# Performance work log

Hardware: AMD Instinct MI355X
Metric: run time of the kernel (lower is better)

## Reference

```python
import jax, jax.numpy as jnp
import numpy as np

M, L = 256, 256
E_EDGES = L - 1
EPS = 1e-12
HX, HZ, JZ = 3.0, 0.25, -1.0


def setup_inputs() -> dict:
    key = jax.random.key(0)
    k1, k2 = jax.random.split(key, 2)
    # original: uniform(-pi/2, pi/2); narrowed to keep cos(theta_m - theta_b) away from 0
    theta = jax.random.uniform(k1, (M, L), minval=-0.3, maxval=0.3, dtype=jnp.float32)
    coef = jax.random.uniform(k2, (M,), minval=-1.0, maxval=1.0, dtype=jnp.float32)
    edges_u = jnp.arange(E_EDGES, dtype=jnp.int32)       # 1D chain
    edges_v = edges_u + 1
    strengths = jnp.ones((E_EDGES,), dtype=jnp.float32)
    return {"theta": theta, "coef": coef, "edges_u": edges_u,
            "edges_v": edges_v, "strengths": strengths}


def reference(theta, coef, edges_u, edges_v, strengths):
    # theta: [M, L], coef: [M]
    cos_m = jnp.cos(theta)
    sin_m = jnp.sin(theta)
    cm = cos_m[:, None, :]   # [M,1,L] -> row m
    sm = sin_m[:, None, :]
    cb = cos_m[None, :, :]   # [1,M,L] -> row b
    sb = sin_m[None, :, :]
    # pairwise angle-sum/difference trig, all [M, M, L]
    cosd = cm * cb + sm * sb            # cos(theta_m - theta_b)
    sind = sm * cb - cm * sb            # sin(theta_m - theta_b)
    sins = sm * cb + cm * sb            # sin(theta_m + theta_b)
    coss = cm * cb - sm * sb            # cos(theta_m + theta_b)
    inv = 1.0 / (cosd + EPS)

    P = jnp.prod(cosd, axis=-1)                     # [M,M] overlap products
    U = jnp.sum(sins * inv, axis=-1)                # [M,M] sigma_x amplitude ratios
    V = jnp.sum(coss * inv, axis=-1)                # [M,M] sigma_z amplitude ratios
    a = coss * inv                                  # [M,M,L] per-site z ratio

    # ZZ interaction over graph edges
    Szz = jnp.einsum('e,mbe->mb', strengths,
                     a[:, :, edges_u] * a[:, :, edges_v])  # [M,M]

    F_total = HZ * V + HX * U + JZ * Szz            # [M,M]
    base = coef[:, None] * coef[None, :] * P        # [M,M]
    N = jnp.sum(base * F_total)
    D = jnp.sum(base)

    cP = coef[None, :] * P                          # c_b * P
    dN_dc = 2.0 * jnp.sum(cP * F_total, axis=1)     # [M]
    dD_dc = 2.0 * jnp.sum(cP, axis=1)               # [M]

    g_d = -sind * inv                               # d log cosd / d theta_mq
    Gxz = (-HZ * sins + HX * coss) * inv + (HZ * coss + HX * sins) * (sind * inv * inv)

    # incident-edge neighbor sums: inc[m,b,q] = sum_{e incident to q} s_e * a[m,b,nbr]
    uu = jnp.concatenate([edges_u, edges_v])
    vv = jnp.concatenate([edges_v, edges_u])
    ss = jnp.concatenate([strengths, strengths])
    inc = jnp.zeros_like(a).at[:, :, uu].add(ss * a[:, :, vv])
    Gzz = (-sins * inv + coss * (sind * inv * inv)) * inc * JZ

    w = base[:, :, None]                            # [M,M,1]
    dD_dtheta = 2.0 * jnp.sum(w * g_d, axis=1)      # [M,L]
    dN_dtheta = 2.0 * jnp.sum(
        w * (g_d * F_total[:, :, None] + Gxz + Gzz), axis=1)  # [M,L]

    E = N / D
    dE_dc = (dN_dc - E * dD_dc) / D
    dE_dtheta = (dN_dtheta - E * dD_dtheta) / D
    return dE_dtheta, dE_dc, E / L
```

## Files before the change

kernel.cpp:

```cpp
#include <hip/hip_runtime.h>
#include <math.h>

#define HXc 3.0f
#define HZc 0.25f
#define JZc (-1.0f)

#define OFF_COSR 0
#define OFF_SINR 65536
#define OFF_COST 131072
#define OFF_SINT 196608
#define OFF_DNT  262144
#define OFF_DDT  327680
#define OFF_NM   393216
#define OFF_DM   393472
#define OFF_CN   393728
#define OFF_CD   393984

__global__ __launch_bounds__(256) void k_prep(const float* __restrict__ theta,
                                              float* __restrict__ ws) {
    int i = blockIdx.x * 256 + threadIdx.x;
    float s, c;
    sincosf(theta[i], &s, &c);
    int m = i >> 8, l = i & 255;
    ws[OFF_COSR + i] = c;
    ws[OFF_SINR + i] = s;
    ws[OFF_COST + l * 256 + m] = c;
    ws[OFF_SINT + l * 256 + m] = s;
}

__global__ __launch_bounds__(1024) void k_main(
        const float* __restrict__ coef,
        const float* __restrict__ strengths,
        const float* __restrict__ cosR, const float* __restrict__ sinR,
        const float* __restrict__ cosT, const float* __restrict__ sinT,
        float* __restrict__ dNT, float* __restrict__ dDT,
        float* __restrict__ Nm, float* __restrict__ Dm,
        float* __restrict__ cN, float* __restrict__ cD) {
    int m = blockIdx.x;
    int tid = threadIdx.x;
    float coefm = coef[m];

    __shared__ float sLDS[256];
    __shared__ float4 quart[4][256];
    __shared__ float Flds[256], cPlds[256];
    __shared__ float wr[4][4];
    __shared__ float gN[16 * 256];
    __shared__ float gD[16 * 256];

    if (tid < 256) sLDS[tid] = (tid < 255) ? strengths[tid] : 0.0f;
    __syncthreads();

    {
        int b = tid & 255, q = tid >> 8;
        int l0 = q * 64;
        float p = 1.0f, u = 0.0f, v = 0.0f, z = 0.0f, a_prev = 0.0f;
        if (q) {
            int l = l0 - 1;
            float cmv = cosT[l * 256 + m], smv = sinT[l * 256 + m];
            float cbv = cosT[l * 256 + b], sbv = sinT[l * 256 + b];
            float t1 = cmv * cbv, t2 = smv * sbv;
            a_prev = (t1 - t2) * __builtin_amdgcn_rcpf(t1 + t2);
        }
        for (int l = l0; l < l0 + 64; ++l) {
            float cmv = cosT[l * 256 + m], smv = sinT[l * 256 + m];
            float cbv = cosT[l * 256 + b], sbv = sinT[l * 256 + b];
            float t1 = cmv * cbv, t2 = smv * sbv;
            float t3 = smv * cbv, t4 = cmv * sbv;
            float cosd = t1 + t2;
            float coss = t1 - t2;
            float sins = t3 + t4;
            float inv = __builtin_amdgcn_rcpf(cosd);
            p *= cosd;
            u = fmaf(sins, inv, u);
            v = fmaf(coss, inv, v);
            float a = coss * inv;
            float sPrev = (l > 0) ? sLDS[l - 1] : 0.0f;
            z = fmaf(sPrev * a_prev, a, z);
            a_prev = a;
        }
        quart[q][b] = make_float4(p, u, v, z);
    }
    __syncthreads();

    if (tid < 256) {
        float4 A = quart[0][tid], B = quart[1][tid];
        float4 C = quart[2][tid], Dq = quart[3][tid];
        float P = A.x * B.x * C.x * Dq.x;
        float U = A.y + B.y + C.y + Dq.y;
        float V = A.z + B.z + C.z + Dq.z;
        float Z = A.w + B.w + C.w + Dq.w;
        float F = HZc * V + HXc * U + JZc * Z;
        float cP = coef[tid] * P;
        Flds[tid] = F;
        cPlds[tid] = cP;
        float base = coefm * cP;
        float s1 = base, s2 = base * F, s3 = cP, s4 = cP * F;
        for (int o = 32; o; o >>= 1) {
            s1 += __shfl_xor(s1, o);
            s2 += __shfl_xor(s2, o);
            s3 += __shfl_xor(s3, o);
            s4 += __shfl_xor(s4, o);
        }
        if ((tid & 63) == 0) {
            int w = tid >> 6;
            wr[w][0] = s1; wr[w][1] = s2; wr[w][2] = s3; wr[w][3] = s4;
        }
    }
    __syncthreads();
    if (tid == 0) {
        Dm[m] = wr[0][0] + wr[1][0] + wr[2][0] + wr[3][0];
        Nm[m] = wr[0][1] + wr[1][1] + wr[2][1] + wr[3][1];
        cD[m] = wr[0][2] + wr[1][2] + wr[2][2] + wr[3][2];
        cN[m] = wr[0][3] + wr[1][3] + wr[2][3] + wr[3][3];
    }

    int w = tid >> 6, lane = tid & 63;
    int l0 = lane * 4;
    float4 cm4 = *(const float4*)&cosR[m * 256 + l0];
    float4 sm4 = *(const float4*)&sinR[m * 256 + l0];
    float cmv[4] = {cm4.x, cm4.y, cm4.z, cm4.w};
    float smv[4] = {sm4.x, sm4.y, sm4.z, sm4.w};
    float sR[4], sL[4];
#pragma unroll
    for (int j = 0; j < 4; ++j) {
        int l = l0 + j;
        sR[j] = sLDS[l];
        sL[j] = (l > 0) ? sLDS[l - 1] : 0.0f;
    }
    float pN[4] = {0.f, 0.f, 0.f, 0.f};
    float pD[4] = {0.f, 0.f, 0.f, 0.f};

    for (int i = 0; i < 16; ++i) {
        int b = w * 16 + i;
        float4 cb4 = *(const float4*)&cosR[b * 256 + l0];
        float4 sb4 = *(const float4*)&sinR[b * 256 + l0];
        float cbv[4] = {cb4.x, cb4.y, cb4.z, cb4.w};
        float sbv[4] = {sb4.x, sb4.y, sb4.z, sb4.w};
        float Fv = Flds[b];
        float base = coefm * cPlds[b];

        float a[4], inv[4], coss[4], sins[4], sind[4];
#pragma unroll
        for (int j = 0; j < 4; ++j) {
            float t1 = cmv[j] * cbv[j], t2 = smv[j] * sbv[j];
            float t3 = smv[j] * cbv[j], t4 = cmv[j] * sbv[j];
            float cosd = t1 + t2;
            coss[j] = t1 - t2;
            sins[j] = t3 + t4;
            sind[j] = t3 - t4;
            inv[j] = __builtin_amdgcn_rcpf(cosd);
            a[j] = coss[j] * inv[j];
        }
        float aLn = __shfl_up(a[3], 1);
        if (lane == 0) aLn = 0.0f;
        float aRn = __shfl_down(a[0], 1);
        if (lane == 63) aRn = 0.0f;
        float am1[4] = {aLn, a[0], a[1], a[2]};
        float ap1[4] = {a[1], a[2], a[3], aRn};
#pragma unroll
        for (int j = 0; j < 4; ++j) {
            float sii = sind[j] * inv[j];
            float g_d = -sii;
            float Gxz = (HXc * coss[j] - HZc * sins[j]) * inv[j]
                      + (HZc * coss[j] + HXc * sins[j]) * (sii * inv[j]);
            float K = JZc * ((coss[j] * sii - sins[j]) * inv[j]);
            float inc = fmaf(sR[j], ap1[j], sL[j] * am1[j]);
            float term = fmaf(Fv, g_d, fmaf(K, inc, Gxz));
            pN[j] = fmaf(base, term, pN[j]);
            pD[j] = fmaf(base, g_d, pD[j]);
        }
    }

    ((float4*)gN)[w * 64 + lane] = make_float4(pN[0], pN[1], pN[2], pN[3]);
    ((float4*)gD)[w * 64 + lane] = make_float4(pD[0], pD[1], pD[2], pD[3]);
    __syncthreads();
    if (tid < 256) {
        float sn = 0.0f, sd = 0.0f;
#pragma unroll
        for (int ww = 0; ww < 16; ++ww) {
            sn += gN[ww * 256 + tid];
            sd += gD[ww * 256 + tid];
        }
        dNT[m * 256 + tid] = sn;
        dDT[m * 256 + tid] = sd;
    }
}

__global__ __launch_bounds__(256) void k_fin(const float* __restrict__ ws,
                                             float* __restrict__ out) {
    int m = blockIdx.x, t = threadIdx.x;
    float nv = ws[OFF_NM + t], dv = ws[OFF_DM + t];
    for (int o = 32; o; o >>= 1) {
        nv += __shfl_xor(nv, o);
        dv += __shfl_xor(dv, o);
    }
    __shared__ float rn[4], rd[4];
    if ((t & 63) == 0) { rn[t >> 6] = nv; rd[t >> 6] = dv; }
    __syncthreads();
    float N = rn[0] + rn[1] + rn[2] + rn[3];
    float D = rd[0] + rd[1] + rd[2] + rd[3];
    float E = N / D;
    float invD = 1.0f / D;
    int i = m * 256 + t;
    out[i] = 2.0f * invD * (ws[OFF_DNT + i] - E * ws[OFF_DDT + i]);
    if (t == 0) out[65536 + m] = 2.0f * invD * (ws[OFF_CN + m] - E * ws[OFF_CD + m]);
    if (m == 0 && t == 1) out[65792] = E * (1.0f / 256.0f);
}

extern "C" void kernel_launch(void* const* d_in, const int* in_sizes, int n_in,
                              void* d_out, int out_size, void* d_ws, size_t ws_size,
                              hipStream_t stream) {
    const float* theta = (const float*)d_in[0];
    const float* coef = (const float*)d_in[1];
    const float* strengths = (const float*)d_in[4];
    float* out = (float*)d_out;
    float* ws = (float*)d_ws;

    k_prep<<<256, 256, 0, stream>>>(theta, ws);
    k_main<<<256, 1024, 0, stream>>>(coef, strengths,
                                     ws + OFF_COSR, ws + OFF_SINR,
                                     ws + OFF_COST, ws + OFF_SINT,
                                     ws + OFF_DNT, ws + OFF_DDT,
                                     ws + OFF_NM, ws + OFF_DM,
                                     ws + OFF_CN, ws + OFF_CD);
    k_fin<<<256, 256, 0, stream>>>(ws, out);
}
```

Baseline: 98.48 us.

## Fuse prep, main and finalize kernels into one cooperative kernel with grid syncs

Merges the three launches (sincos prep, main pairwise accumulation, final normalisation) into a single cooperative kernel that uses grid.sync between phases. Per-block gradient partials and c-gradient scalars now stay in LDS instead of round-tripping through workspace. This removes two kernel launch gaps and some global traffic. In exchange it adds the cost of grid-wide barriers and requires all 256 blocks of 1024 threads to be co-resident. It also reuses a = coss*inv for the V sum.

```diff
diff --git a/kernel.cpp b/kernel.cpp
--- a/kernel.cpp
+++ b/kernel.cpp
@@ -1,5 +1,8 @@
 #include <hip/hip_runtime.h>
+#include <hip/hip_cooperative_groups.h>
 #include <math.h>
+
+namespace cg = cooperative_groups;
 
 #define HXc 3.0f
 #define HZc 0.25f
@@ -9,36 +12,26 @@
 #define OFF_SINR 65536
 #define OFF_COST 131072
 #define OFF_SINT 196608
-#define OFF_DNT  262144
-#define OFF_DDT  327680
-#define OFF_NM   393216
-#define OFF_DM   393472
-#define OFF_CN   393728
-#define OFF_CD   393984
-
-__global__ __launch_bounds__(256) void k_prep(const float* __restrict__ theta,
-                                              float* __restrict__ ws) {
-    int i = blockIdx.x * 256 + threadIdx.x;
-    float s, c;
-    sincosf(theta[i], &s, &c);
-    int m = i >> 8, l = i & 255;
-    ws[OFF_COSR + i] = c;
-    ws[OFF_SINR + i] = s;
-    ws[OFF_COST + l * 256 + m] = c;
-    ws[OFF_SINT + l * 256 + m] = s;
-}
-
-__global__ __launch_bounds__(1024) void k_main(
+#define OFF_NM   262144
+#define OFF_DM   262400
+
+__global__ __launch_bounds__(1024) void k_all(
+        const float* __restrict__ theta,
         const float* __restrict__ coef,
         const float* __restrict__ strengths,
-        const float* __restrict__ cosR, const float* __restrict__ sinR,
-        const float* __restrict__ cosT, const float* __restrict__ sinT,
-        float* __restrict__ dNT, float* __restrict__ dDT,
-        float* __restrict__ Nm, float* __restrict__ Dm,
-        float* __restrict__ cN, float* __restrict__ cD) {
+        float* __restrict__ ws,
+        float* __restrict__ out) {
+    cg::grid_group grid = cg::this_grid();
+
     int m = blockIdx.x;
     int tid = threadIdx.x;
-    float coefm = coef[m];
+
+    float* __restrict__ cosR = ws + OFF_COSR;
+    float* __restrict__ sinR = ws + OFF_SINR;
+    float* __restrict__ cosT = ws + OFF_COST;
+    float* __restrict__ sinT = ws + OFF_SINT;
+    float* __restrict__ Nm = ws + OFF_NM;
+    float* __restrict__ Dm = ws + OFF_DM;
 
     __shared__ float sLDS[256];
     __shared__ float4 quart[4][256];
@@ -46,9 +39,20 @@
     __shared__ float wr[4][4];
     __shared__ float gN[16 * 256];
     __shared__ float gD[16 * 256];
-
-    if (tid < 256) sLDS[tid] = (tid < 255) ? strengths[tid] : 0.0f;
-    __syncthreads();
+    __shared__ float snL[256], sdL[256];
+    __shared__ float scal[4];
+
+    if (tid < 256) {
+        sLDS[tid] = (tid < 255) ? strengths[tid] : 0.0f;
+        int i = m * 256 + tid;
+        float s, c;
+        sincosf(theta[i], &s, &c);
+        cosR[i] = c;
+        sinR[i] = s;
+        cosT[tid * 256 + m] = c;
+        sinT[tid * 256 + m] = s;
+    }
+    grid.sync();
 
     {
         int b = tid & 255, q = tid >> 8;
@@ -72,8 +76,8 @@
             float inv = __builtin_amdgcn_rcpf(cosd);
             p *= cosd;
             u = fmaf(sins, inv, u);
-            v = fmaf(coss, inv, v);
             float a = coss * inv;
+            v += a;
             float sPrev = (l > 0) ? sLDS[l - 1] : 0.0f;
             z = fmaf(sPrev * a_prev, a, z);
             a_prev = a;
@@ -93,6 +97,7 @@
         float cP = coef[tid] * P;
         Flds[tid] = F;
         cPlds[tid] = cP;
+        float coefm = coef[m];
         float base = coefm * cP;
         float s1 = base, s2 = base * F, s3 = cP, s4 = cP * F;
         for (int o = 32; o; o >>= 1) {
@@ -110,69 +115,71 @@
     if (tid == 0) {
         Dm[m] = wr[0][0] + wr[1][0] + wr[2][0] + wr[3][0];
         Nm[m] = wr[0][1] + wr[1][1] + wr[2][1] + wr[3][1];
-        cD[m] = wr[0][2] + wr[1][2] + wr[2][2] + wr[3][2];
-        cN[m] = wr[0][3] + wr[1][3] + wr[2][3] + wr[3][3];
-    }
-
-    int w = tid >> 6, lane = tid & 63;
-    int l0 = lane * 4;
-    float4 cm4 = *(const float4*)&cosR[m * 256 + l0];
-    float4 sm4 = *(const float4*)&sinR[m * 256 + l0];
-    float cmv[4] = {cm4.x, cm4.y, cm4.z, cm4.w};
-    float smv[4] = {sm4.x, sm4.y, sm4.z, sm4.w};
-    float sR[4], sL[4];
-#pragma unroll
-    for (int j = 0; j < 4; ++j) {
-        int l = l0 + j;
-        sR[j] = sLDS[l];
-        sL[j] = (l > 0) ? sLDS[l - 1] : 0.0f;
-    }
-    float pN[4] = {0.f, 0.f, 0.f, 0.f};
-    float pD[4] = {0.f, 0.f, 0.f, 0.f};
-
-    for (int i = 0; i < 16; ++i) {
-        int b = w * 16 + i;
-        float4 cb4 = *(const float4*)&cosR[b * 256 + l0];
-        float4 sb4 = *(const float4*)&sinR[b * 256 + l0];
-        float cbv[4] = {cb4.x, cb4.y, cb4.z, cb4.w};
-        float sbv[4] = {sb4.x, sb4.y, sb4.z, sb4.w};
-        float Fv = Flds[b];
-        float base = coefm * cPlds[b];
-
-        float a[4], inv[4], coss[4], sins[4], sind[4];
+        scal[1] = wr[0][2] + wr[1][2] + wr[2][2] + wr[3][2];
+        scal[0] = wr[0][3] + wr[1][3] + wr[2][3] + wr[3][3];
+    }
+
+    {
+        int w = tid >> 6, lane = tid & 63;
+        int l0 = lane * 4;
+        float coefm = coef[m];
+        float4 cm4 = *(const float4*)&cosR[m * 256 + l0];
+        float4 sm4 = *(const float4*)&sinR[m * 256 + l0];
+        float cmv[4] = {cm4.x, cm4.y, cm4.z, cm4.w};
+        float smv[4] = {sm4.x, sm4.y, sm4.z, sm4.w};
+        float sR[4], sL[4];
 #pragma unroll
         for (int j = 0; j < 4; ++j) {
-            float t1 = cmv[j] * cbv[j], t2 = smv[j] * sbv[j];
-            float t3 = smv[j] * cbv[j], t4 = cmv[j] * sbv[j];
-            float cosd = t1 + t2;
-            coss[j] = t1 - t2;
-            sins[j] = t3 + t4;
-            sind[j] = t3 - t4;
-            inv[j] = __builtin_amdgcn_rcpf(cosd);
-            a[j] = coss[j] * inv[j];
-        }
-        float aLn = __shfl_up(a[3], 1);
-        if (lane == 0) aLn = 0.0f;
-        float aRn = __shfl_down(a[0], 1);
-        if (lane == 63) aRn = 0.0f;
-        float am1[4] = {aLn, a[0], a[1], a[2]};
-        float ap1[4] = {a[1], a[2], a[3], aRn};
-#pragma unroll
-        for (int j = 0; j < 4; ++j) {
-            float sii = sind[j] * inv[j];
-            float g_d = -sii;
-            float Gxz = (HXc * coss[j] - HZc * sins[j]) * inv[j]
-                      + (HZc * coss[j] + HXc * sins[j]) * (sii * inv[j]);
-            float K = JZc * ((coss[j] * sii - sins[j]) * inv[j]);
-            float inc = fmaf(sR[j], ap1[j], sL[j] * am1[j]);
-            float term = fmaf(Fv, g_d, fmaf(K, inc, Gxz));
-            pN[j] = fmaf(base, term, pN[j]);
-            pD[j] = fmaf(base, g_d, pD[j]);
-        }
-    }
-
-    ((float4*)gN)[w * 64 + lane] = make_float4(pN[0], pN[1], pN[2], pN[3]);
-    ((float4*)gD)[w * 64 + lane] = make_float4(pD[0], pD[1], pD[2], pD[3]);
+            int l = l0 + j;
+            sR[j] = sLDS[l];
+            sL[j] = (l > 0) ? sLDS[l - 1] : 0.0f;
+        }
+        float pN[4] = {0.f, 0.f, 0.f, 0.f};
+        float pD[4] = {0.f, 0.f, 0.f, 0.f};
+
+        for (int i = 0; i < 16; ++i) {
+            int b = w * 16 + i;
+            float4 cb4 = *(const float4*)&cosR[b * 256 + l0];
+            float4 sb4 = *(const float4*)&sinR[b * 256 + l0];
+            float cbv[4] = {cb4.x, cb4.y, cb4.z, cb4.w};
+            float sbv[4] = {sb4.x, sb4.y, sb4.z, sb4.w};
+            float Fv = Flds[b];
+            float base = coefm * cPlds[b];
+
+            float a[4], inv[4], coss[4], sins[4], sind[4];
+#pragma unroll
+            for (int j = 0; j < 4; ++j) {
+                float t1 = cmv[j] * cbv[j], t2 = smv[j] * sbv[j];
+                float t3 = smv[j] * cbv[j], t4 = cmv[j] * sbv[j];
+                float cosd = t1 + t2;
+                coss[j] = t1 - t2;
+                sins[j] = t3 + t4;
+                sind[j] = t3 - t4;
+                inv[j] = __builtin_amdgcn_rcpf(cosd);
+                a[j] = coss[j] * inv[j];
+            }
+            float aLn = __shfl_up(a[3], 1);
+            if (lane == 0) aLn = 0.0f;
+            float aRn = __shfl_down(a[0], 1);
+            if (lane == 63) aRn = 0.0f;
+            float am1[4] = {aLn, a[0], a[1], a[2]};
+            float ap1[4] = {a[1], a[2], a[3], aRn};
+#pragma unroll
+            for (int j = 0; j < 4; ++j) {
+                float sii = sind[j] * inv[j];
+                float g_d = -sii;
+                float Gxz = (HXc * coss[j] - HZc * sins[j]) * inv[j]
+                          + (HZc * coss[j] + HXc * sins[j]) * (sii * inv[j]);
+                float K = JZc * ((coss[j] * sii - sins[j]) * inv[j]);
+                float inc = fmaf(sR[j], ap1[j], sL[j] * am1[j]);
+                float term = fmaf(Fv, g_d, fmaf(K, inc, Gxz));
+                pN[j] = fmaf(base, term, pN[j]);
+                pD[j] = fmaf(base, g_d, pD[j]);
+            }
+        }
+        ((float4*)gN)[w * 64 + lane] = make_float4(pN[0], pN[1], pN[2], pN[3]);
+        ((float4*)gD)[w * 64 + lane] = make_float4(pD[0], pD[1], pD[2], pD[3]);
+    }
     __syncthreads();
     if (tid < 256) {
         float sn = 0.0f, sd = 0.0f;
@@ -181,30 +188,41 @@
             sn += gN[ww * 256 + tid];
             sd += gD[ww * 256 + tid];
         }
-        dNT[m * 256 + tid] = sn;
-        dDT[m * 256 + tid] = sd;
-    }
-}
-
-__global__ __launch_bounds__(256) void k_fin(const float* __restrict__ ws,
-                                             float* __restrict__ out) {
-    int m = blockIdx.x, t = threadIdx.x;
-    float nv = ws[OFF_NM + t], dv = ws[OFF_DM + t];
-    for (int o = 32; o; o >>= 1) {
-        nv += __shfl_xor(nv, o);
-        dv += __shfl_xor(dv, o);
-    }
-    __shared__ float rn[4], rd[4];
-    if ((t & 63) == 0) { rn[t >> 6] = nv; rd[t >> 6] = dv; }
-    __syncthreads();
-    float N = rn[0] + rn[1] + rn[2] + rn[3];
-    float D = rd[0] + rd[1] + rd[2] + rd[3];
-    float E = N / D;
-    float invD = 1.0f / D;
-    int i = m * 256 + t;
-    out[i] = 2.0f * invD * (ws[OFF_DNT + i] - E * ws[OFF_DDT + i]);
-    if (t == 0) out[65536 + m] = 2.0f * invD * (ws[OFF_CN + m] - E * ws[OFF_CD + m]);
-    if (m == 0 && t == 1) out[65792] = E * (1.0f / 256.0f);
+        snL[tid] = sn;
+        sdL[tid] = sd;
+    }
+    __threadfence();
+    grid.sync();
+
+    if (tid < 256) {
+        float nv = Nm[tid], dv = Dm[tid];
+        for (int o = 32; o; o >>= 1) {
+            nv += __shfl_xor(nv, o);
+            dv += __shfl_xor(dv, o);
+        }
+        if ((tid & 63) == 0) {
+            int w = tid >> 6;
+            wr[w][0] = nv; wr[w][1] = dv;
+        }
+    }
+    __syncthreads();
+    if (tid == 0) {
+        float N = wr[0][0] + wr[1][0] + wr[2][0] + wr[3][0];
+        float D = wr[0][1] + wr[1][1] + wr[2][1] + wr[3][1];
+        scal[2] = N / D;
+        scal[3] = 1.0f / D;
+    }
+    __syncthreads();
+    float E = scal[2], invD = scal[3];
+    if (tid < 256) {
+        out[m * 256 + tid] = 2.0f * invD * (snL[tid] - E * sdL[tid]);
+    }
+    if (tid == 0) {
+        out[65536 + m] = 2.0f * invD * (scal[0] - E * scal[1]);
+    }
+    if (m == 0 && tid == 1) {
+        out[65792] = E * (1.0f / 256.0f);
+    }
 }
 
 extern "C" void kernel_launch(void* const* d_in, const int* in_sizes, int n_in,
@@ -216,12 +234,8 @@
     float* out = (float*)d_out;
     float* ws = (float*)d_ws;
 
-    k_prep<<<256, 256, 0, stream>>>(theta, ws);
-    k_main<<<256, 1024, 0, stream>>>(coef, strengths,
-                                     ws + OFF_COSR, ws + OFF_SINR,
-                                     ws + OFF_COST, ws + OFF_SINT,
-                                     ws + OFF_DNT, ws + OFF_DDT,
-                                     ws + OFF_NM, ws + OFF_DM,
-                                     ws + OFF_CN, ws + OFF_CD);
-    k_fin<<<256, 256, 0, stream>>>(ws, out);
+    void* args[] = {(void*)&theta, (void*)&coef, (void*)&strengths,
+                    (void*)&ws, (void*)&out};
+    hipLaunchCooperativeKernel((const void*)k_all, dim3(256), dim3(1024),
+                               args, 0, stream);
 }
```

Measured after the change: 232.2 us. 136% more time.

## Reformulate pairwise trig in tangent form and precompute per-row cosine products

Applied to the files above, without the earlier changes.

Replaces the cos/sin pair representation with tan(theta). Every pairwise ratio (cos sum over cos difference, sin sum over cos difference, sin difference over cos difference) then becomes a rational function of tm*tb, and the overlap product is split into per-row cosine products times the product of (1+tm*tb). This halves global loads, drops the transposed cos/sin buffers, and removes several multiplies per element in both passes. The m-row tangents are also staged in LDS. The risk is precision: the per-row cosine product over 256 sites and the 256-term product of (1+q) are accumulated separately, which could drift or underflow for other inputs.

```diff
diff --git a/kernel.cpp b/kernel.cpp
--- a/kernel.cpp
+++ b/kernel.cpp
@@ -5,87 +5,87 @@
 #define HZc 0.25f
 #define JZc (-1.0f)
 
-#define OFF_COSR 0
-#define OFF_SINR 65536
-#define OFF_COST 131072
-#define OFF_SINT 196608
-#define OFF_DNT  262144
-#define OFF_DDT  327680
-#define OFF_NM   393216
-#define OFF_DM   393472
-#define OFF_CN   393728
-#define OFF_CD   393984
+#define OFF_TANR 0
+#define OFF_TANT 65536
+#define OFF_CPR  131072
+#define OFF_DNT  131328
+#define OFF_DDT  196864
+#define OFF_NM   262400
+#define OFF_DM   262656
+#define OFF_CN   262912
+#define OFF_CD   263168
 
 __global__ __launch_bounds__(256) void k_prep(const float* __restrict__ theta,
                                               float* __restrict__ ws) {
-    int i = blockIdx.x * 256 + threadIdx.x;
+    int m = blockIdx.x, t = threadIdx.x;
     float s, c;
-    sincosf(theta[i], &s, &c);
-    int m = i >> 8, l = i & 255;
-    ws[OFF_COSR + i] = c;
-    ws[OFF_SINR + i] = s;
-    ws[OFF_COST + l * 256 + m] = c;
-    ws[OFF_SINT + l * 256 + m] = s;
+    sincosf(theta[m * 256 + t], &s, &c);
+    float tn = s / c;
+    ws[OFF_TANR + m * 256 + t] = tn;
+    ws[OFF_TANT + t * 256 + m] = tn;
+    float pr = c;
+    for (int o = 32; o; o >>= 1) pr *= __shfl_xor(pr, o);
+    __shared__ float pp[4];
+    if ((t & 63) == 0) pp[t >> 6] = pr;
+    __syncthreads();
+    if (t == 0) ws[OFF_CPR + m] = pp[0] * pp[1] * pp[2] * pp[3];
 }
 
 __global__ __launch_bounds__(1024) void k_main(
         const float* __restrict__ coef,
         const float* __restrict__ strengths,
-        const float* __restrict__ cosR, const float* __restrict__ sinR,
-        const float* __restrict__ cosT, const float* __restrict__ sinT,
-        float* __restrict__ dNT, float* __restrict__ dDT,
-        float* __restrict__ Nm, float* __restrict__ Dm,
-        float* __restrict__ cN, float* __restrict__ cD) {
+        float* __restrict__ ws) {
     int m = blockIdx.x;
     int tid = threadIdx.x;
-    float coefm = coef[m];
+    const float* __restrict__ tanR = ws + OFF_TANR;
+    const float* __restrict__ tanT = ws + OFF_TANT;
+    const float* __restrict__ Cpr = ws + OFF_CPR;
 
     __shared__ float sLDS[256];
+    __shared__ float tmL[256];
     __shared__ float4 quart[4][256];
     __shared__ float Flds[256], cPlds[256];
     __shared__ float wr[4][4];
     __shared__ float gN[16 * 256];
     __shared__ float gD[16 * 256];
 
-    if (tid < 256) sLDS[tid] = (tid < 255) ? strengths[tid] : 0.0f;
+    if (tid < 256) {
+        sLDS[tid] = (tid < 255) ? strengths[tid] : 0.0f;
+        tmL[tid] = tanR[m * 256 + tid];
+    }
     __syncthreads();
 
     {
         int b = tid & 255, q = tid >> 8;
         int l0 = q * 64;
-        float p = 1.0f, u = 0.0f, v = 0.0f, z = 0.0f, a_prev = 0.0f;
+        float pw = 1.0f, u = 0.0f, v = 0.0f, z = 0.0f, a_prev = 0.0f;
         if (q) {
             int l = l0 - 1;
-            float cmv = cosT[l * 256 + m], smv = sinT[l * 256 + m];
-            float cbv = cosT[l * 256 + b], sbv = sinT[l * 256 + b];
-            float t1 = cmv * cbv, t2 = smv * sbv;
-            a_prev = (t1 - t2) * __builtin_amdgcn_rcpf(t1 + t2);
+            float qq = tmL[l] * tanT[l * 256 + b];
+            a_prev = (1.0f - qq) * __builtin_amdgcn_rcpf(1.0f + qq);
         }
         for (int l = l0; l < l0 + 64; ++l) {
-            float cmv = cosT[l * 256 + m], smv = sinT[l * 256 + m];
-            float cbv = cosT[l * 256 + b], sbv = sinT[l * 256 + b];
-            float t1 = cmv * cbv, t2 = smv * sbv;
-            float t3 = smv * cbv, t4 = cmv * sbv;
-            float cosd = t1 + t2;
-            float coss = t1 - t2;
-            float sins = t3 + t4;
-            float inv = __builtin_amdgcn_rcpf(cosd);
-            p *= cosd;
-            u = fmaf(sins, inv, u);
-            v = fmaf(coss, inv, v);
-            float a = coss * inv;
+            float tm = tmL[l];
+            float tb = tanT[l * 256 + b];
+            float qq = tm * tb;
+            float w1 = 1.0f + qq;
+            float inv = __builtin_amdgcn_rcpf(w1);
+            pw *= w1;
+            u = fmaf(tm + tb, inv, u);
+            float a = (1.0f - qq) * inv;
+            v += a;
             float sPrev = (l > 0) ? sLDS[l - 1] : 0.0f;
             z = fmaf(sPrev * a_prev, a, z);
             a_prev = a;
         }
-        quart[q][b] = make_float4(p, u, v, z);
+        quart[q][b] = make_float4(pw, u, v, z);
     }
     __syncthreads();
 
     if (tid < 256) {
         float4 A = quart[0][tid], B = quart[1][tid];
         float4 C = quart[2][tid], Dq = quart[3][tid];
-        float P = A.x * B.x * C.x * Dq.x;
+        float P = Cpr[m] * Cpr[tid] * (A.x * B.x * C.x * Dq.x);
         float U = A.y + B.y + C.y + Dq.y;
         float V = A.z + B.z + C.z + Dq.z;
         float Z = A.w + B.w + C.w + Dq.w;
@@ -93,7 +93,7 @@
         float cP = coef[tid] * P;
         Flds[tid] = F;
         cPlds[tid] = cP;
-        float base = coefm * cP;
+        float base = coef[m] * cP;
         float s1 = base, s2 = base * F, s3 = cP, s4 = cP * F;
         for (int o = 32; o; o >>= 1) {
             s1 += __shfl_xor(s1, o);
@@ -108,71 +108,65 @@
     }
     __syncthreads();
     if (tid == 0) {
-        Dm[m] = wr[0][0] + wr[1][0] + wr[2][0] + wr[3][0];
-        Nm[m] = wr[0][1] + wr[1][1] + wr[2][1] + wr[3][1];
-        cD[m] = wr[0][2] + wr[1][2] + wr[2][2] + wr[3][2];
-        cN[m] = wr[0][3] + wr[1][3] + wr[2][3] + wr[3][3];
-    }
-
-    int w = tid >> 6, lane = tid & 63;
-    int l0 = lane * 4;
-    float4 cm4 = *(const float4*)&cosR[m * 256 + l0];
-    float4 sm4 = *(const float4*)&sinR[m * 256 + l0];
-    float cmv[4] = {cm4.x, cm4.y, cm4.z, cm4.w};
-    float smv[4] = {sm4.x, sm4.y, sm4.z, sm4.w};
-    float sR[4], sL[4];
-#pragma unroll
-    for (int j = 0; j < 4; ++j) {
-        int l = l0 + j;
-        sR[j] = sLDS[l];
-        sL[j] = (l > 0) ? sLDS[l - 1] : 0.0f;
-    }
-    float pN[4] = {0.f, 0.f, 0.f, 0.f};
-    float pD[4] = {0.f, 0.f, 0.f, 0.f};
-
-    for (int i = 0; i < 16; ++i) {
-        int b = w * 16 + i;
-        float4 cb4 = *(const float4*)&cosR[b * 256 + l0];
-        float4 sb4 = *(const float4*)&sinR[b * 256 + l0];
-        float cbv[4] = {cb4.x, cb4.y, cb4.z, cb4.w};
-        float sbv[4] = {sb4.x, sb4.y, sb4.z, sb4.w};
-        float Fv = Flds[b];
-        float base = coefm * cPlds[b];
-
-        float a[4], inv[4], coss[4], sins[4], sind[4];
+        ws[OFF_DM + m] = wr[0][0] + wr[1][0] + wr[2][0] + wr[3][0];
+        ws[OFF_NM + m] = wr[0][1] + wr[1][1] + wr[2][1] + wr[3][1];
+        ws[OFF_CD + m] = wr[0][2] + wr[1][2] + wr[2][2] + wr[3][2];
+        ws[OFF_CN + m] = wr[0][3] + wr[1][3] + wr[2][3] + wr[3][3];
+    }
+
+    {
+        int w = tid >> 6, lane = tid & 63;
+        int l0 = lane * 4;
+        float coefm = coef[m];
+        float4 tm4 = *(const float4*)&tmL[l0];
+        float tm[4] = {tm4.x, tm4.y, tm4.z, tm4.w};
+        float sR[4], sL[4];
 #pragma unroll
         for (int j = 0; j < 4; ++j) {
-            float t1 = cmv[j] * cbv[j], t2 = smv[j] * sbv[j];
-            float t3 = smv[j] * cbv[j], t4 = cmv[j] * sbv[j];
-            float cosd = t1 + t2;
-            coss[j] = t1 - t2;
-            sins[j] = t3 + t4;
-            sind[j] = t3 - t4;
-            inv[j] = __builtin_amdgcn_rcpf(cosd);
-            a[j] = coss[j] * inv[j];
-        }
-        float aLn = __shfl_up(a[3], 1);
-        if (lane == 0) aLn = 0.0f;
-        float aRn = __shfl_down(a[0], 1);
-        if (lane == 63) aRn = 0.0f;
-        float am1[4] = {aLn, a[0], a[1], a[2]};
-        float ap1[4] = {a[1], a[2], a[3], aRn};
-#pragma unroll
-        for (int j = 0; j < 4; ++j) {
-            float sii = sind[j] * inv[j];
-            float g_d = -sii;
-            float Gxz = (HXc * coss[j] - HZc * sins[j]) * inv[j]
-                      + (HZc * coss[j] + HXc * sins[j]) * (sii * inv[j]);
-            float K = JZc * ((coss[j] * sii - sins[j]) * inv[j]);
-            float inc = fmaf(sR[j], ap1[j], sL[j] * am1[j]);
-            float term = fmaf(Fv, g_d, fmaf(K, inc, Gxz));
-            pN[j] = fmaf(base, term, pN[j]);
-            pD[j] = fmaf(base, g_d, pD[j]);
-        }
-    }
-
-    ((float4*)gN)[w * 64 + lane] = make_float4(pN[0], pN[1], pN[2], pN[3]);
-    ((float4*)gD)[w * 64 + lane] = make_float4(pD[0], pD[1], pD[2], pD[3]);
+            int l = l0 + j;
+            sR[j] = sLDS[l];
+            sL[j] = (l > 0) ? sLDS[l - 1] : 0.0f;
+        }
+        float pN[4] = {0.f, 0.f, 0.f, 0.f};
+        float pD[4] = {0.f, 0.f, 0.f, 0.f};
+
+        for (int i = 0; i < 16; ++i) {
+            int b = w * 16 + i;
+            float4 tb4 = *(const float4*)&tanR[b * 256 + l0];
+            float tb[4] = {tb4.x, tb4.y, tb4.z, tb4.w};
+            float Fv = Flds[b];
+            float base = coefm * cPlds[b];
+
+            float A[4], S[4], G[4];
+#pragma unroll
+            for (int j = 0; j < 4; ++j) {
+                float qq = tm[j] * tb[j];
+                float w1 = 1.0f + qq;
+                float inv = __builtin_amdgcn_rcpf(w1);
+                A[j] = (1.0f - qq) * inv;
+                S[j] = (tm[j] + tb[j]) * inv;
+                G[j] = (tm[j] - tb[j]) * inv;
+            }
+            float aLn = __shfl_up(A[3], 1);
+            if (lane == 0) aLn = 0.0f;
+            float aRn = __shfl_down(A[0], 1);
+            if (lane == 63) aRn = 0.0f;
+            float am1[4] = {aLn, A[0], A[1], A[2]};
+            float ap1[4] = {A[1], A[2], A[3], aRn};
+#pragma unroll
+            for (int j = 0; j < 4; ++j) {
+                float Gxz = fmaf(HXc, A[j], -HZc * S[j])
+                          + fmaf(HZc, A[j], HXc * S[j]) * G[j];
+                float K = JZc * fmaf(A[j], G[j], -S[j]);
+                float inc = fmaf(sR[j], ap1[j], sL[j] * am1[j]);
+                float term = fmaf(Fv, -G[j], fmaf(K, inc, Gxz));
+                pN[j] = fmaf(base, term, pN[j]);
+                pD[j] = fmaf(base, -G[j], pD[j]);
+            }
+        }
+        ((float4*)gN)[w * 64 + lane] = make_float4(pN[0], pN[1], pN[2], pN[3]);
+        ((float4*)gD)[w * 64 + lane] = make_float4(pD[0], pD[1], pD[2], pD[3]);
+    }
     __syncthreads();
     if (tid < 256) {
         float sn = 0.0f, sd = 0.0f;
@@ -181,8 +175,8 @@
             sn += gN[ww * 256 + tid];
             sd += gD[ww * 256 + tid];
         }
-        dNT[m * 256 + tid] = sn;
-        dDT[m * 256 + tid] = sd;
+        ws[OFF_DNT + m * 256 + tid] = sn;
+        ws[OFF_DDT + m * 256 + tid] = sd;
     }
 }
 
@@ -217,11 +211,6 @@
     float* ws = (float*)d_ws;
 
     k_prep<<<256, 256, 0, stream>>>(theta, ws);
-    k_main<<<256, 1024, 0, stream>>>(coef, strengths,
-                                     ws + OFF_COSR, ws + OFF_SINR,
-                                     ws + OFF_COST, ws + OFF_SINT,
-                                     ws + OFF_DNT, ws + OFF_DDT,
-                                     ws + OFF_NM, ws + OFF_DM,
-                                     ws + OFF_CN, ws + OFF_CD);
+    k_main<<<256, 1024, 0, stream>>>(coef, strengths, ws);
     k_fin<<<256, 256, 0, stream>>>(ws, out);
 }
```

Result: faster. 87.94 us (-10.7%).
